# Optimization experiments

Measured on AMD Instinct MI355X. Metric: run time of the kernel, lower is better.

Reference implementation:

```python
import jax, jax.numpy as jnp
import numpy as np

B, H, O, D = 1024, 256, 128, 64
LN_EPS = 1e-6  # flax LayerNorm default


def _layer_norm(h, scale, bias):
    mu = jnp.mean(h, axis=-1, keepdims=True)
    var = jnp.mean((h - mu) ** 2, axis=-1, keepdims=True)
    return (h - mu) * jax.lax.rsqrt(var + LN_EPS) * scale + bias


def _readout(hm, ln_scale, ln_bias, Wout, bout):
    return _layer_norm(hm, ln_scale, ln_bias) @ Wout + bout


def setup_inputs() -> dict:
    key = jax.random.key(0)
    ks = jax.random.split(key, 16)
    n = jax.random.normal
    s_i = 1.0 / np.sqrt(D)
    s_h = 1.0 / np.sqrt(H)
    return {
        # forward args (batched over B independent sequences)
        "x": n(ks[0], (B, D)),
        "y": n(ks[1], (B, O)),
        "m": jnp.ones((B, O), jnp.float32),
        "h": n(ks[2], (B, H)) * 0.1,
        "delta": n(ks[3], (B, H)) * 0.1,
        "inst_delta": n(ks[4], (B, H)) * 0.1,
        "prod_jac": n(ks[5], (B, H, H)) * 0.05,
        "prev_mean": n(ks[6], (B, H)) * 0.1,
        "t": jnp.zeros((B,), jnp.float32),
        # GRU params (flax Dense kernels are [in, out])
        "Wiz": n(ks[7], (D, H)) * s_i, "biz": jnp.zeros((H,)),
        "Whz": n(ks[8], (H, H)) * s_h,
        "Wir": n(ks[9], (D, H)) * s_i, "bir": jnp.zeros((H,)),
        "Whr": n(ks[10], (H, H)) * s_h,
        "Win": n(ks[11], (D, H)) * s_i, "bin_": jnp.zeros((H,)),
        "Whn": n(ks[12], (H, H)) * s_h, "bhn": jnp.zeros((H,)),
        # readout params
        "ln_scale": jnp.ones((H,)), "ln_bias": jnp.zeros((H,)),
        "Wout": n(ks[13], (H, O)) * s_h, "bout": jnp.zeros((O,)),
    }


def reference(x, y, m, h, delta, inst_delta, prod_jac, prev_mean, t,
              Wiz, biz, Whz, Wir, bir, Whr, Win, bin_, Whn, bhn,
              ln_scale, ln_bias, Wout, bout):
    # --- GRU recurrence ---
    r = jax.nn.sigmoid(x @ Wir + bir + h @ Whr)
    z = jax.nn.sigmoid(x @ Wiz + biz + h @ Whz)
    g = h @ Whn + bhn
    n_ = jnp.tanh(x @ Win + bin_ + r * g)
    new_h = (1.0 - z) * n_ + z * h

    new_t = t + 1.0
    new_mean = new_h  # pooling == 'none'
    out = _readout(new_mean, ln_scale, ln_bias, Wout, bout)

    # --- analytic d new_h / d h  (== jax.jacfwd(recurrence, 0)) ---
    dz = z * (1.0 - z)
    dr = r * (1.0 - r)
    dn = 1.0 - n_ * n_
    # J[b,i,j] = d new_h_i / d h_j
    J = (((h - n_) * dz)[:, :, None] * Whz.T
         + ((1.0 - z) * dn * r)[:, :, None] * Whn.T
         + ((1.0 - z) * dn * g * dr)[:, :, None] * Whr.T
         + z[:, :, None] * jnp.eye(H, dtype=z.dtype))
    jac = jnp.swapaxes(J, -1, -2)  # module transposes the jacfwd output

    new_prod_jac = jnp.einsum('bij,bjk->bik', prod_jac, jac)
    # exact inverse path (approx_inverse=False)
    new_delta = jnp.einsum('bij,bj->bi', jnp.linalg.inv(jac), delta - inst_delta)

    # inst_delta = grad of masked-MSE loss wrt new_mean through the readout
    ro = lambda hm: _readout(hm, ln_scale, ln_bias, Wout, bout)
    o2, vjp = jax.vjp(ro, new_mean)
    g_o = 2.0 * m * (o2 - y)  # dL/do for L = sum(m*(o-y)^2)
    (new_inst_delta,) = vjp(g_o)

    delta_output = 2.0 * m * (out - y)
    h_norm = jnp.linalg.norm(new_h, axis=-1)
    delta_norm = jnp.linalg.norm(new_delta, axis=-1)
    prod_jac_norm = jnp.sqrt(jnp.sum(new_prod_jac ** 2, axis=(-2, -1)))

    return (new_h, new_delta, new_inst_delta, new_prod_jac, new_mean, new_t,
            out, h, delta_output, h_norm, delta_norm, prod_jac_norm, jac)
```

## Files before the change

### kernel.cpp

```cpp
#include <hip/hip_runtime.h>
#include <hip/hip_bf16.h>

#define B_N 1024
#define H_N 256
#define O_N 128
#define D_N 64

#define OFF_NEWH      0
#define OFF_NEWDELTA  262144
#define OFF_NEWINST   524288
#define OFF_NEWPJ     786432
#define OFF_NEWMEAN   67895296
#define OFF_NEWT      68157440
#define OFF_OUT       68158464
#define OFF_HCOPY     68289536
#define OFF_DELTAOUT  68551680
#define OFF_HNORM     68682752
#define OFF_DNORM     68683776
#define OFF_PJNORM    68684800
#define OFF_JAC       68685824

typedef __attribute__((ext_vector_type(8))) short short8;
typedef __attribute__((ext_vector_type(4))) float f32x4;

__device__ __forceinline__ short f2bf(float f){
  union { float f; unsigned u; } v; v.f = f;
  unsigned r = v.u + 0x7fffu + ((v.u >> 16) & 1u);
  return (short)(r >> 16);
}

__device__ __forceinline__ float wave_reduce_sum(float v){
  #pragma unroll
  for (int off = 32; off > 0; off >>= 1) v += __shfl_xor(v, off);
  return v;
}

__global__ __launch_bounds__(256) void gates_kernel(
    const float* __restrict__ x, const float* __restrict__ h, const float* __restrict__ tt,
    const float* __restrict__ Wiz, const float* __restrict__ biz, const float* __restrict__ Whz,
    const float* __restrict__ Wir, const float* __restrict__ bir, const float* __restrict__ Whr,
    const float* __restrict__ Win, const float* __restrict__ bin_, const float* __restrict__ Whn,
    const float* __restrict__ bhn,
    float* __restrict__ dout, float* __restrict__ ws)
{
  int b = blockIdx.x, j = threadIdx.x;
  __shared__ float xs[64];
  __shared__ float hs[256];
  __shared__ float red[4];
  if (j < 64) xs[j] = x[b*64 + j];
  float hj = h[b*256 + j];
  hs[j] = hj;
  __syncthreads();

  float zp = biz[j], rp = bir[j], np = bin_[j], g = bhn[j];
  #pragma unroll 8
  for (int k = 0; k < 64; k++){
    float xv = xs[k];
    zp = fmaf(xv, Wiz[k*256 + j], zp);
    rp = fmaf(xv, Wir[k*256 + j], rp);
    np = fmaf(xv, Win[k*256 + j], np);
  }
  #pragma unroll 8
  for (int k = 0; k < 256; k++){
    float hv = hs[k];
    zp = fmaf(hv, Whz[k*256 + j], zp);
    rp = fmaf(hv, Whr[k*256 + j], rp);
    g  = fmaf(hv, Whn[k*256 + j], g);
  }
  float r = 1.f / (1.f + expf(-rp));
  float z = 1.f / (1.f + expf(-zp));
  float n = tanhf(np + r*g);
  float nh = (1.f - z)*n + z*hj;

  float dz = z*(1.f - z);
  float dn = 1.f - n*n;
  float drv = r*(1.f - r);
  float az = (hj - n)*dz;
  float an = (1.f - z)*dn*r;
  float ar = (1.f - z)*dn*g*drv;

  dout[OFF_NEWH   + b*256 + j] = nh;
  dout[OFF_NEWMEAN+ b*256 + j] = nh;
  dout[OFF_HCOPY  + b*256 + j] = hj;
  ws[0*262144 + b*256 + j] = z;
  ws[1*262144 + b*256 + j] = az;
  ws[2*262144 + b*256 + j] = an;
  ws[3*262144 + b*256 + j] = ar;

  float s = wave_reduce_sum(nh*nh);
  if ((j & 63) == 0) red[j >> 6] = s;
  __syncthreads();
  if (j == 0){
    dout[OFF_HNORM + b] = sqrtf(red[0] + red[1] + red[2] + red[3]);
    dout[OFF_NEWT + b] = tt[b] + 1.f;
  }
}

__global__ __launch_bounds__(1024, 4) void solve_kernel(
    const float* __restrict__ Whz, const float* __restrict__ Whn, const float* __restrict__ Whr,
    const float* __restrict__ ws, const float* __restrict__ delta,
    const float* __restrict__ inst_delta, float* __restrict__ dout)
{
  const int b = blockIdx.x, tid = threadIdx.x;
  const int l  = tid & 63;
  const int w  = tid >> 6;
  const int wr = w >> 2, wc = w & 3;
  const int lr = l >> 3, lc = l & 7;
  const int r0 = wr*64 + lr*8;
  const int c0 = wc*64 + lc*8;

  __shared__ __align__(16) float DT[2][8*264];
  __shared__ __align__(16) float RB[8*264];
  __shared__ __align__(16) float rhs[256];
  __shared__ __align__(16) float pivval_s[256];
  __shared__ int   perm_s[256];

  float A[8][8];
  {
    float* jac_out = dout + OFF_JAC + (size_t)b*65536;
    #pragma unroll
    for (int half = 0; half < 2; half++){
      const int cb = c0 + half*4;
      float4 vz4 = *(const float4*)(ws + 0*262144 + b*256 + cb);
      float4 va4 = *(const float4*)(ws + 1*262144 + b*256 + cb);
      float4 vn4 = *(const float4*)(ws + 2*262144 + b*256 + cb);
      float4 vr4 = *(const float4*)(ws + 3*262144 + b*256 + cb);
      float zc[4] = {vz4.x, vz4.y, vz4.z, vz4.w};
      float az[4] = {va4.x, va4.y, va4.z, va4.w};
      float an[4] = {vn4.x, vn4.y, vn4.z, vn4.w};
      float ar[4] = {vr4.x, vr4.y, vr4.z, vr4.w};
      #pragma unroll
      for (int i = 0; i < 8; i++){
        const int row = r0 + i;
        float4 wz = *(const float4*)(Whz + row*256 + cb);
        float4 wn = *(const float4*)(Whn + row*256 + cb);
        float4 wq = *(const float4*)(Whr + row*256 + cb);
        A[i][half*4+0] = fmaf(wz.x, az[0], fmaf(wn.x, an[0], wq.x*ar[0]));
        A[i][half*4+1] = fmaf(wz.y, az[1], fmaf(wn.y, an[1], wq.y*ar[1]));
        A[i][half*4+2] = fmaf(wz.z, az[2], fmaf(wn.z, an[2], wq.z*ar[2]));
        A[i][half*4+3] = fmaf(wz.w, az[3], fmaf(wn.w, an[3], wq.w*ar[3]));
        #pragma unroll
        for (int k = 0; k < 4; k++)
          if (cb + k == row) A[i][half*4+k] += zc[k];
        *(float4*)(jac_out + row*256 + cb) =
            make_float4(A[i][half*4+0], A[i][half*4+1], A[i][half*4+2], A[i][half*4+3]);
      }
    }
  }

  if (tid < 256) rhs[tid] = delta[b*256 + tid] - inst_delta[b*256 + tid];

  if (wc == 0 && lc == 0){
    #pragma unroll
    for (int c = 0; c < 8; c++){
      *(float4*)&DT[0][c*264 + r0]     = make_float4(A[0][c], A[1][c], A[2][c], A[3][c]);
      *(float4*)&DT[0][c*264 + r0 + 4] = make_float4(A[4][c], A[5][c], A[6][c], A[7][c]);
    }
  }
  unsigned usedbits = 0u;
  __syncthreads();

  for (int kb = 0; kb < 32; kb++){
    const int cur = kb & 1;
    float* __restrict__ Dc = &DT[cur][0];
    float* __restrict__ Dn = &DT[cur ^ 1][0];

    if (w == 0){
      float4 curc = *(const float4*)&Dc[0*264 + 4*l];
      #pragma unroll
      for (int j = 0; j < 8; j++){
        float c4[4] = {curc.x, curc.y, curc.z, curc.w};
        unsigned key = 0u;
        #pragma unroll
        for (int q = 0; q < 4; q++){
          unsigned kq = (__float_as_uint(fabsf(c4[q])) & 0xFFFFFF00u) | (unsigned)(l*4 + q);
          bool fresh = ((usedbits >> q) & 1u) == 0u;
          key = (fresh && kq > key) ? kq : key;
        }
        #pragma unroll
        for (int off = 32; off > 0; off >>= 1){
          unsigned ok = __shfl_xor(key, off);
          key = ok > key ? ok : key;
        }
        const int p = (int)(key & 255u);
        float sel = c4[0];
        #pragma unroll
        for (int q = 1; q < 4; q++) sel = ((p & 3) == q) ? c4[q] : sel;
        const float pv = __shfl(sel, p >> 2);
        const float ipv = 1.0f / pv;
        if ((p >> 2) == l) usedbits |= 1u << (p & 3);
        const bool own = ((p >> 2) == l);
        float d4[4];
        #pragma unroll
        for (int q = 0; q < 4; q++){
          float dv = c4[q] * ipv;
          d4[q] = (own && (p & 3) == q) ? 0.f : dv;
        }
        float prow[8];
        #pragma unroll
        for (int c = 0; c < 8; c++) prow[c] = Dc[c*264 + p];
        #pragma unroll
        for (int c = 0; c < 8; c++){
          if (c == j){
            *(float4*)&Dc[j*264 + 4*l] = make_float4(d4[0], d4[1], d4[2], d4[3]);
          } else {
            float4 pc = *(const float4*)&Dc[c*264 + 4*l];
            pc.x = fmaf(-d4[0], prow[c], pc.x);
            pc.y = fmaf(-d4[1], prow[c], pc.y);
            pc.z = fmaf(-d4[2], prow[c], pc.z);
            pc.w = fmaf(-d4[3], prow[c], pc.w);
            if (c == j + 1) curc = pc;
            else *(float4*)&Dc[c*264 + 4*l] = pc;
          }
        }
        if (l == 0){ perm_s[kb*8 + j] = p; pivval_s[kb*8 + j] = pv; }
      }
    }
    __syncthreads();

    int pq8[8];
    #pragma unroll
    for (int q = 0; q < 8; q++) pq8[q] = perm_s[kb*8 + q];
    #pragma unroll
    for (int i = 0; i < 8; i++){
      int qm = -1;
      #pragma unroll
      for (int q = 0; q < 8; q++) qm = (pq8[q] == r0 + i) ? q : qm;
      if (qm >= 0){
        *(float4*)&RB[qm*264 + c0]     = make_float4(A[i][0], A[i][1], A[i][2], A[i][3]);
        *(float4*)&RB[qm*264 + c0 + 4] = make_float4(A[i][4], A[i][5], A[i][6], A[i][7]);
      }
    }
    float rhsP[8];
    if (tid < 256){
      #pragma unroll
      for (int q = 0; q < 8; q++) rhsP[q] = rhs[pq8[q]];
    }
    __syncthreads();

    if (kb < 31){
      #pragma unroll 1
      for (int q = 0; q < 8; q++){
        float4 d0 = *(const float4*)&Dc[q*264 + r0];
        float4 d1 = *(const float4*)&Dc[q*264 + r0 + 4];
        float4 ra = *(const float4*)&RB[q*264 + c0];
        float4 rb4 = *(const float4*)&RB[q*264 + c0 + 4];
        float dq[8] = {d0.x, d0.y, d0.z, d0.w, d1.x, d1.y, d1.z, d1.w};
        float rq[8] = {ra.x, ra.y, ra.z, ra.w, rb4.x, rb4.y, rb4.z, rb4.w};
        #pragma unroll
        for (int i = 0; i < 8; i++)
          #pragma unroll
          for (int j = 0; j < 8; j++)
            A[i][j] = fmaf(-dq[i], rq[j], A[i][j]);
      }
      if (wc == ((kb+1) >> 3) && lc == ((kb+1) & 7)){
        #pragma unroll
        for (int c = 0; c < 8; c++){
          *(float4*)&Dn[c*264 + r0]     = make_float4(A[0][c], A[1][c], A[2][c], A[3][c]);
          *(float4*)&Dn[c*264 + r0 + 4] = make_float4(A[4][c], A[5][c], A[6][c], A[7][c]);
        }
      }
    }
    if (tid < 256){
      float rv = rhs[tid];
      #pragma unroll 1
      for (int q = 0; q < 8; q++) rv = fmaf(-Dc[q*264 + tid], rhsP[q], rv);
      rhs[tid] = rv;
    }
    __syncthreads();
  }

  if (tid < 256){
    float xv = rhs[perm_s[tid]] / pivval_s[tid];
    dout[OFF_NEWDELTA + b*256 + tid] = xv;
    RB[tid] = xv*xv;
  }
  __syncthreads();
  if (tid < 64){
    float s = RB[tid] + RB[tid+64] + RB[tid+128] + RB[tid+192];
    s = wave_reduce_sum(s);
    if (tid == 0) dout[OFF_DNORM + b] = sqrtf(s);
  }
}

__global__ __launch_bounds__(512) void pj_gemm_kernel(
    const float* __restrict__ prod_jac, const float* __restrict__ jac,
    float* __restrict__ out_pj, float* __restrict__ out_norm)
{
  int b = blockIdx.x, tid = threadIdx.x;
  int l = tid & 63, wid = tid >> 6;
  int wm = wid >> 2, wn = wid & 3;
  int lr = l & 15, lg = l >> 4;

  __shared__ float As[256*33];
  __shared__ float Bs[256*33];

  const float* Ag = prod_jac + (size_t)b*65536;
  const float* Bg = jac      + (size_t)b*65536;

  f32x4 acc[8][4];
  #pragma unroll
  for (int i = 0; i < 8; i++)
    #pragma unroll
    for (int jn = 0; jn < 4; jn++) acc[i][jn] = (f32x4){0.f,0.f,0.f,0.f};

  const int arow = tid >> 1, acolb = (tid & 1)*16;
  const int bk = tid >> 4, bcolb = (tid & 15)*16;

  for (int kt = 0; kt < 8; ++kt){
    const int k0 = kt*32;
    __syncthreads();
    {
      const float4* asrc = (const float4*)(Ag + arow*256 + k0 + acolb);
      float* ad = &As[arow*33 + acolb];
      #pragma unroll
      for (int q = 0; q < 4; q++){
        float4 v = asrc[q];
        ad[q*4+0]=v.x; ad[q*4+1]=v.y; ad[q*4+2]=v.z; ad[q*4+3]=v.w;
      }
      const float4* bsrc = (const float4*)(Bg + (k0 + bk)*256 + bcolb);
      #pragma unroll
      for (int q = 0; q < 4; q++){
        float4 v = bsrc[q];
        Bs[(bcolb+q*4+0)*33 + bk] = v.x;
        Bs[(bcolb+q*4+1)*33 + bk] = v.y;
        Bs[(bcolb+q*4+2)*33 + bk] = v.z;
        Bs[(bcolb+q*4+3)*33 + bk] = v.w;
      }
    }
    __syncthreads();

    short8 bfr[4];
    #pragma unroll
    for (int ni = 0; ni < 4; ni++){
      const float* bp = &Bs[(wn*64 + ni*16 + lr)*33 + lg*8];
      short8 t;
      #pragma unroll
      for (int v = 0; v < 8; v++) t[v] = f2bf(bp[v]);
      bfr[ni] = t;
    }
    #pragma unroll
    for (int mi = 0; mi < 8; mi++){
      const float* ap = &As[(wm*128 + mi*16 + lr)*33 + lg*8];
      short8 af;
      #pragma unroll
      for (int v = 0; v < 8; v++) af[v] = f2bf(ap[v]);
      #pragma unroll
      for (int ni = 0; ni < 4; ni++)
        acc[mi][ni] = __builtin_amdgcn_mfma_f32_16x16x32_bf16(af, bfr[ni], acc[mi][ni], 0, 0, 0);
    }
  }

  float nrm = 0.f;
  #pragma unroll
  for (int mi = 0; mi < 8; mi++){
    #pragma unroll
    for (int ni = 0; ni < 4; ni++){
      #pragma unroll
      for (int rr = 0; rr < 4; rr++){
        int row = wm*128 + mi*16 + lg*4 + rr;
        int col = wn*64 + ni*16 + lr;
        float vv = acc[mi][ni][rr];
        out_pj[(size_t)b*65536 + row*256 + col] = vv;
        nrm += vv*vv;
      }
    }
  }
  __syncthreads();
  As[tid] = nrm;
  __syncthreads();
  if (tid < 64){
    float s = 0.f;
    #pragma unroll
    for (int q = 0; q < 8; q++) s += As[tid + q*64];
    s = wave_reduce_sum(s);
    if (tid == 0) out_norm[b] = sqrtf(s);
  }
}

__global__ __launch_bounds__(256) void readout_kernel(
    const float* __restrict__ y, const float* __restrict__ m,
    const float* __restrict__ ln_scale, const float* __restrict__ ln_bias,
    const float* __restrict__ Wout, const float* __restrict__ bout,
    float* __restrict__ dout)
{
  int b = blockIdx.x, j = threadIdx.x;
  __shared__ float lno[256], xh[256], go[128], red2[256], red[4];

  float hv = dout[OFF_NEWH + b*256 + j];
  float s = wave_reduce_sum(hv);
  if ((j & 63) == 0) red[j >> 6] = s;
  __syncthreads();
  float mu = (red[0] + red[1] + red[2] + red[3]) * (1.f/256.f);
  __syncthreads();
  float d = hv - mu;
  float sv = wave_reduce_sum(d*d);
  if ((j & 63) == 0) red[j >> 6] = sv;
  __syncthreads();
  float var = (red[0] + red[1] + red[2] + red[3]) * (1.f/256.f);
  float rstd = rsqrtf(var + 1e-6f);
  float xhj = d * rstd;
  xh[j] = xhj;
  lno[j] = xhj * ln_scale[j] + ln_bias[j];
  __syncthreads();

  int i = j & 127, half = j >> 7;
  float part = half ? 0.f : bout[i];
  #pragma unroll 8
  for (int jj = half*128; jj < half*128 + 128; jj++)
    part = fmaf(lno[jj], Wout[jj*128 + i], part);
  red2[j] = part;
  __syncthreads();
  if (j < 128){
    float o = red2[j] + red2[j + 128];
    float gv = 2.f * m[b*128 + j] * (o - y[b*128 + j]);
    dout[OFF_OUT + b*128 + j] = o;
    dout[OFF_DELTAOUT + b*128 + j] = gv;
    go[j] = gv;
  }
  __syncthreads();

  float gl = 0.f;
  const float4* wrow = (const float4*)(Wout + j*128);
  #pragma unroll 8
  for (int q = 0; q < 32; q++){
    float4 w = wrow[q];
    gl = fmaf(w.x, go[q*4+0], gl);
    gl = fmaf(w.y, go[q*4+1], gl);
    gl = fmaf(w.z, go[q*4+2], gl);
    gl = fmaf(w.w, go[q*4+3], gl);
  }
  float gx = gl * ln_scale[j];
  __syncthreads();
  float t1 = wave_reduce_sum(gx);
  if ((j & 63) == 0) red[j >> 6] = t1;
  __syncthreads();
  float s1 = (red[0] + red[1] + red[2] + red[3]) * (1.f/256.f);
  __syncthreads();
  float t2 = wave_reduce_sum(gx * xhj);
  if ((j & 63) == 0) red[j >> 6] = t2;
  __syncthreads();
  float s2m = (red[0] + red[1] + red[2] + red[3]) * (1.f/256.f);
  float nid = rstd * (gx - s1 - xhj * s2m);
  dout[OFF_NEWINST + b*256 + j] = nid;
}

extern "C" void kernel_launch(void* const* d_in, const int* in_sizes, int n_in,
                              void* d_out, int out_size, void* d_ws, size_t ws_size,
                              hipStream_t stream) {
  const float* x          = (const float*)d_in[0];
  const float* y          = (const float*)d_in[1];
  const float* m          = (const float*)d_in[2];
  const float* h          = (const float*)d_in[3];
  const float* delta      = (const float*)d_in[4];
  const float* inst_delta = (const float*)d_in[5];
  const float* prod_jac   = (const float*)d_in[6];
  const float* t          = (const float*)d_in[8];
  const float* Wiz  = (const float*)d_in[9];
  const float* biz  = (const float*)d_in[10];
  const float* Whz  = (const float*)d_in[11];
  const float* Wir  = (const float*)d_in[12];
  const float* bir  = (const float*)d_in[13];
  const float* Whr  = (const float*)d_in[14];
  const float* Win  = (const float*)d_in[15];
  const float* bin_ = (const float*)d_in[16];
  const float* Whn  = (const float*)d_in[17];
  const float* bhn  = (const float*)d_in[18];
  const float* ln_scale = (const float*)d_in[19];
  const float* ln_bias  = (const float*)d_in[20];
  const float* Wout = (const float*)d_in[21];
  const float* bout = (const float*)d_in[22];

  float* dout = (float*)d_out;
  float* ws = (float*)d_ws;

  gates_kernel<<<1024, 256, 0, stream>>>(x, h, t, Wiz, biz, Whz, Wir, bir, Whr,
                                         Win, bin_, Whn, bhn, dout, ws);
  solve_kernel<<<1024, 1024, 0, stream>>>(Whz, Whn, Whr, ws, delta, inst_delta, dout);
  pj_gemm_kernel<<<1024, 512, 0, stream>>>(prod_jac, dout + OFF_JAC,
                                           dout + OFF_NEWPJ, dout + OFF_PJNORM);
  readout_kernel<<<1024, 256, 0, stream>>>(y, m, ln_scale, ln_bias, Wout, bout, dout);
}
```

Measured before the change: 1.733 ms.

## Overlap RHS update with pivot search, use DPP wave max, raise pivot-wave priority

Replaces the shuffle-based wave max in the pivot search with a DPP reduction plus readlane, and raises wave 0's scheduling priority during the serial panel factorization. The RHS elimination update is moved to threads 256-511 and deferred one step so it runs alongside the next panel's pivot search instead of after the trailing update, with a final flush after the loop. This shortens the serial critical path per block step, at the cost of needing at least 512 threads and correct double-buffer indexing for the deferred update.

```diff
diff --git a/kernel.cpp b/kernel.cpp
--- a/kernel.cpp
+++ b/kernel.cpp
@@ -33,6 +33,17 @@
   #pragma unroll
   for (int off = 32; off > 0; off >>= 1) v += __shfl_xor(v, off);
   return v;
+}
+
+__device__ __forceinline__ int wave_max_dpp(int v){
+  int t;
+  t = __builtin_amdgcn_update_dpp(v, v, 0x111, 0xf, 0xf, false); v = v > t ? v : t;
+  t = __builtin_amdgcn_update_dpp(v, v, 0x112, 0xf, 0xf, false); v = v > t ? v : t;
+  t = __builtin_amdgcn_update_dpp(v, v, 0x114, 0xf, 0xf, false); v = v > t ? v : t;
+  t = __builtin_amdgcn_update_dpp(v, v, 0x118, 0xf, 0xf, false); v = v > t ? v : t;
+  t = __builtin_amdgcn_update_dpp(v, v, 0x142, 0xf, 0xf, false); v = v > t ? v : t;
+  t = __builtin_amdgcn_update_dpp(v, v, 0x143, 0xf, 0xf, false); v = v > t ? v : t;
+  return __builtin_amdgcn_readlane(v, 63);
 }
 
 __global__ __launch_bounds__(256) void gates_kernel(
@@ -158,6 +169,7 @@
     }
   }
   unsigned usedbits = 0u;
+  float rhsP[8];
   __syncthreads();
 
   for (int kb = 0; kb < 32; kb++){
@@ -166,6 +178,7 @@
     float* __restrict__ Dn = &DT[cur ^ 1][0];
 
     if (w == 0){
+      __builtin_amdgcn_s_setprio(1);
       float4 curc = *(const float4*)&Dc[0*264 + 4*l];
       #pragma unroll
       for (int j = 0; j < 8; j++){
@@ -177,12 +190,7 @@
           bool fresh = ((usedbits >> q) & 1u) == 0u;
           key = (fresh && kq > key) ? kq : key;
         }
-        #pragma unroll
-        for (int off = 32; off > 0; off >>= 1){
-          unsigned ok = __shfl_xor(key, off);
-          key = ok > key ? ok : key;
-        }
-        const int p = (int)(key & 255u);
+        const int p = wave_max_dpp((int)key) & 255;
         float sel = c4[0];
         #pragma unroll
         for (int q = 1; q < 4; q++) sel = ((p & 3) == q) ? c4[q] : sel;
@@ -215,6 +223,14 @@
         }
         if (l == 0){ perm_s[kb*8 + j] = p; pivval_s[kb*8 + j] = pv; }
       }
+      __builtin_amdgcn_s_setprio(0);
+    }
+    if (kb > 0 && tid >= 256 && tid < 512){
+      const int e = tid - 256;
+      float rv = rhs[e];
+      #pragma unroll 1
+      for (int q = 0; q < 8; q++) rv = fmaf(-Dn[q*264 + e], rhsP[q], rv);
+      rhs[e] = rv;
     }
     __syncthreads();
 
@@ -231,8 +247,7 @@
         *(float4*)&RB[qm*264 + c0 + 4] = make_float4(A[i][4], A[i][5], A[i][6], A[i][7]);
       }
     }
-    float rhsP[8];
-    if (tid < 256){
+    if (tid >= 256 && tid < 512){
       #pragma unroll
       for (int q = 0; q < 8; q++) rhsP[q] = rhs[pq8[q]];
     }
@@ -261,14 +276,17 @@
         }
       }
     }
-    if (tid < 256){
-      float rv = rhs[tid];
-      #pragma unroll 1
-      for (int q = 0; q < 8; q++) rv = fmaf(-Dc[q*264 + tid], rhsP[q], rv);
-      rhs[tid] = rv;
-    }
     __syncthreads();
   }
+
+  if (tid >= 256 && tid < 512){
+    const int e = tid - 256;
+    float rv = rhs[e];
+    #pragma unroll 1
+    for (int q = 0; q < 8; q++) rv = fmaf(-DT[1][q*264 + e], rhsP[q], rv);
+    rhs[e] = rv;
+  }
+  __syncthreads();
 
   if (tid < 256){
     float xv = rhs[perm_s[tid]] / pivval_s[tid];
```

New measurement: 1.611 ms (median of 2 runs). 7.0% less time.

## Spread pivot-panel factorization across all waves with DPP max reduction

Applied to the files above, without the earlier changes.

The panel LU step (pivot search and elimination over an 8-column panel) used to run on wave 0 alone, with each lane handling 4 rows. Now every wave holds one row per lane in registers. The pivot is found with a DPP wave-max, followed by a cross-wave reduction through shared memory and block barriers. The aim is to cut the serial work per pivot and stop the other 15 waves from idling, at the cost of two __syncthreads per pivot column.

```diff
diff --git a/kernel.cpp b/kernel.cpp
--- a/kernel.cpp
+++ b/kernel.cpp
@@ -33,6 +33,17 @@
   #pragma unroll
   for (int off = 32; off > 0; off >>= 1) v += __shfl_xor(v, off);
   return v;
+}
+
+__device__ __forceinline__ int wave_max_dpp(int v){
+  int t;
+  t = __builtin_amdgcn_update_dpp(v, v, 0x111, 0xf, 0xf, false); v = v > t ? v : t;
+  t = __builtin_amdgcn_update_dpp(v, v, 0x112, 0xf, 0xf, false); v = v > t ? v : t;
+  t = __builtin_amdgcn_update_dpp(v, v, 0x114, 0xf, 0xf, false); v = v > t ? v : t;
+  t = __builtin_amdgcn_update_dpp(v, v, 0x118, 0xf, 0xf, false); v = v > t ? v : t;
+  t = __builtin_amdgcn_update_dpp(v, v, 0x142, 0xf, 0xf, false); v = v > t ? v : t;
+  t = __builtin_amdgcn_update_dpp(v, v, 0x143, 0xf, 0xf, false); v = v > t ? v : t;
+  return __builtin_amdgcn_readlane(v, 63);
 }
 
 __global__ __launch_bounds__(256) void gates_kernel(
@@ -108,12 +119,15 @@
   const int lr = l >> 3, lc = l & 7;
   const int r0 = wr*64 + lr*8;
   const int c0 = wc*64 + lc*8;
+  const int rowp = wr*64 + l;
 
   __shared__ __align__(16) float DT[2][8*264];
   __shared__ __align__(16) float RB[8*264];
   __shared__ __align__(16) float rhs[256];
   __shared__ __align__(16) float pivval_s[256];
   __shared__ int   perm_s[256];
+  __shared__ int   scanb[16];
+  __shared__ float prowb[8];
 
   float A[8][8];
   {
@@ -157,7 +171,7 @@
       *(float4*)&DT[0][c*264 + r0 + 4] = make_float4(A[4][c], A[5][c], A[6][c], A[7][c]);
     }
   }
-  unsigned usedbits = 0u;
+  bool used = false;
   __syncthreads();
 
   for (int kb = 0; kb < 32; kb++){
@@ -165,56 +179,44 @@
     float* __restrict__ Dc = &DT[cur][0];
     float* __restrict__ Dn = &DT[cur ^ 1][0];
 
-    if (w == 0){
-      float4 curc = *(const float4*)&Dc[0*264 + 4*l];
-      #pragma unroll
-      for (int j = 0; j < 8; j++){
-        float c4[4] = {curc.x, curc.y, curc.z, curc.w};
-        unsigned key = 0u;
+    float P[8];
+    #pragma unroll
+    for (int c = 0; c < 8; c++) P[c] = Dc[c*264 + rowp];
+    #pragma unroll 1
+    for (int j = 0; j < 8; j++){
+      unsigned key = used ? 0u
+          : ((__float_as_uint(fabsf(P[j])) & 0xFFFFFF00u) | (unsigned)rowp);
+      int wmax = wave_max_dpp((int)key);
+      if (l == 0) scanb[w] = wmax;
+      __syncthreads();
+      int g = scanb[0];
+      #pragma unroll
+      for (int i = 1; i < 16; i++){ int sv = scanb[i]; g = sv > g ? sv : g; }
+      const int p = g & 255;
+      if (wc == 0 && rowp == p){
         #pragma unroll
-        for (int q = 0; q < 4; q++){
-          unsigned kq = (__float_as_uint(fabsf(c4[q])) & 0xFFFFFF00u) | (unsigned)(l*4 + q);
-          bool fresh = ((usedbits >> q) & 1u) == 0u;
-          key = (fresh && kq > key) ? kq : key;
-        }
-        #pragma unroll
-        for (int off = 32; off > 0; off >>= 1){
-          unsigned ok = __shfl_xor(key, off);
-          key = ok > key ? ok : key;
-        }
-        const int p = (int)(key & 255u);
-        float sel = c4[0];
-        #pragma unroll
-        for (int q = 1; q < 4; q++) sel = ((p & 3) == q) ? c4[q] : sel;
-        const float pv = __shfl(sel, p >> 2);
-        const float ipv = 1.0f / pv;
-        if ((p >> 2) == l) usedbits |= 1u << (p & 3);
-        const bool own = ((p >> 2) == l);
-        float d4[4];
-        #pragma unroll
-        for (int q = 0; q < 4; q++){
-          float dv = c4[q] * ipv;
-          d4[q] = (own && (p & 3) == q) ? 0.f : dv;
-        }
-        float prow[8];
-        #pragma unroll
-        for (int c = 0; c < 8; c++) prow[c] = Dc[c*264 + p];
-        #pragma unroll
-        for (int c = 0; c < 8; c++){
-          if (c == j){
-            *(float4*)&Dc[j*264 + 4*l] = make_float4(d4[0], d4[1], d4[2], d4[3]);
-          } else {
-            float4 pc = *(const float4*)&Dc[c*264 + 4*l];
-            pc.x = fmaf(-d4[0], prow[c], pc.x);
-            pc.y = fmaf(-d4[1], prow[c], pc.y);
-            pc.z = fmaf(-d4[2], prow[c], pc.z);
-            pc.w = fmaf(-d4[3], prow[c], pc.w);
-            if (c == j + 1) curc = pc;
-            else *(float4*)&Dc[c*264 + 4*l] = pc;
-          }
-        }
-        if (l == 0){ perm_s[kb*8 + j] = p; pivval_s[kb*8 + j] = pv; }
-      }
+        for (int c = 0; c < 8; c++) prowb[c] = P[c];
+      }
+      __syncthreads();
+      float prow[8];
+      #pragma unroll
+      for (int c = 0; c < 8; c++) prow[c] = prowb[c];
+      const float pv = prow[j];
+      const float ipv = 1.0f / pv;
+      const bool own = (rowp == p);
+      if (own) used = true;
+      const float d = own ? 0.f : P[j] * ipv;
+      #pragma unroll
+      for (int c = 0; c < 8; c++){
+        if (c == j) continue;
+        P[c] = fmaf(-d, prow[c], P[c]);
+      }
+      P[j] = d;
+      if (tid == 0){ perm_s[kb*8 + j] = p; pivval_s[kb*8 + j] = pv; }
+    }
+    if (wc == 0){
+      #pragma unroll
+      for (int c = 0; c < 8; c++) Dc[c*264 + rowp] = P[c];
     }
     __syncthreads();
 
```

Measured after the change: 2.472 ms. 1.43x slower.
